# Kernel optimization log

Measured on AMD Instinct MI355X. Metric: run time of the kernel, lower is better.

Reference implementation:

```python
import jax, jax.numpy as jnp
import numpy as np

HIDDEN = 1024
HEADS = 16
CHUNK = 128
NEG_INF = -1e10  # matches source's -10000000000.0


def setup_inputs() -> dict:
    key = jax.random.key(0)
    k1, k2, k3 = jax.random.split(key, 3)
    B, S = 2, 4096
    x = jax.random.normal(k1, (B, S, HIDDEN), dtype=jnp.float32)
    w_qkv = jax.random.normal(k2, (HIDDEN, 3 * HIDDEN), dtype=jnp.float32) / np.sqrt(HIDDEN).astype(np.float32)
    w_out = jax.random.normal(k3, (HIDDEN, HIDDEN), dtype=jnp.float32) / np.sqrt(HIDDEN).astype(np.float32)
    return {"x": x, "w_qkv": w_qkv, "w_out": w_out}


def reference(x, w_qkv, w_out):
    B, S, _ = x.shape
    H, D = HEADS, HIDDEN // HEADS
    # fused qkv projection (flax Dense, no bias): [B,S,3,H,D]
    qkv = (x @ w_qkv).reshape(B, S, 3, H, D)
    q, k, v = qkv[:, :, 0], qkv[:, :, 1], qkv[:, :, 2]
    scale = jnp.sqrt(jnp.asarray(D, x.dtype))
    n_chunks = S // CHUNK
    # [n_chunks, B, CHUNK, H, D] query chunks; scan keeps only one chunk's
    # [B,H,CHUNK,S] score tensor live at a time (faithful to source's chunking).
    q_chunks = q.reshape(B, n_chunks, CHUNK, H, D).transpose(1, 0, 2, 3, 4)
    starts = jnp.arange(n_chunks) * CHUNK

    def step(carry, inp):
        qc, start = inp  # qc: [B,CHUNK,H,D]
        scores = jnp.einsum('bqhd,bkhd->bhqk', qc, k) / scale  # [B,H,CHUNK,S]
        causal = (jnp.arange(CHUNK)[:, None] + start) >= jnp.arange(S)[None, :]
        scores = jnp.where(causal[None, None], scores, NEG_INF)
        attn = jax.nn.softmax(scores, axis=-1)
        out_c = jnp.einsum('bhqk,bkhd->bqhd', attn, v).reshape(B, CHUNK, H * D)
        return carry, out_c

    _, outs = jax.lax.scan(step, None, (q_chunks, starts))  # [n,B,CHUNK,hidden]
    out = outs.transpose(1, 0, 2, 3).reshape(B, S, H * D)
    return out @ w_out
```

## Files before the change

kernel.cpp:

```cpp
#include <hip/hip_runtime.h>
#include <hip/hip_bf16.h>

#define SEQ 4096
#define BATCH 2
#define HEADS 16
#define DHEAD 64
#define HID 1024

typedef unsigned short ushort_t;
typedef unsigned int uint_t;
typedef __attribute__((ext_vector_type(8))) short short8;
typedef __attribute__((ext_vector_type(4))) float f32x4;
typedef __attribute__((ext_vector_type(16))) float f32x16;
typedef __attribute__((ext_vector_type(4))) uint_t u32x4;

__device__ __forceinline__ float exp2_fast(float x) {
  return __builtin_amdgcn_exp2f(x);
}

__device__ __forceinline__ float max3f(float a, float b, float c) {
  float r;
  asm("v_max3_f32 %0, %1, %2, %3" : "=v"(r) : "v"(a), "v"(b), "v"(c));
  return r;
}

__device__ __forceinline__ ushort_t f2b(float f) {
  unsigned u = __builtin_bit_cast(unsigned, f);
  unsigned r = 0x7fffu + ((u >> 16) & 1u);
  return (ushort_t)((u + r) >> 16);
}

__device__ __forceinline__ uint_t cvt_pk_bf16(float lo, float hi) {
  uint_t r;
  asm("v_cvt_pk_bf16_f32 %0, %1, %2" : "=v"(r) : "v"(lo), "v"(hi));
  return r;
}

__device__ __forceinline__ void permlane_swap(uint_t& a, uint_t& b) {
  asm("v_permlane32_swap_b32 %0, %1" : "+v"(a), "+v"(b));
}

__device__ __forceinline__ void gload16(const void* g, void* l) {
  __builtin_amdgcn_global_load_lds((const __attribute__((address_space(1))) void*)g,
                                   (__attribute__((address_space(3))) void*)l, 16, 0, 0);
}

__device__ __forceinline__ f32x4 mfma_bf16(short8 a, short8 b, f32x4 c) {
  return __builtin_amdgcn_mfma_f32_16x16x32_bf16(a, b, c, 0, 0, 0);
}

__device__ __forceinline__ f32x16 mfma32_bf16(short8 a, short8 b, f32x16 c) {
  return __builtin_amdgcn_mfma_f32_32x32x16_bf16(a, b, c, 0, 0, 0);
}

__global__ void cvt_kernel(const float* __restrict__ in, ushort_t* __restrict__ out, int n4) {
  int i = blockIdx.x * blockDim.x + threadIdx.x;
  if (i >= n4) return;
  float4 v = reinterpret_cast<const float4*>(in)[i];
  ushort4 o;
  o.x = f2b(v.x); o.y = f2b(v.y); o.z = f2b(v.z); o.w = f2b(v.w);
  reinterpret_cast<ushort4*>(out)[i] = o;
}

__global__ void transpose_cvt_kernel(const float* __restrict__ in, ushort_t* __restrict__ out,
                                     int rows, int cols) {
  __shared__ float tile[32][33];
  int tx = threadIdx.x & 31, ty = threadIdx.x >> 5;
  int r0 = blockIdx.y * 32, c0 = blockIdx.x * 32;
#pragma unroll
  for (int i = 0; i < 32; i += 8)
    tile[ty + i][tx] = in[(size_t)(r0 + ty + i) * cols + c0 + tx];
  __syncthreads();
#pragma unroll
  for (int i = 0; i < 32; i += 8)
    out[(size_t)(c0 + ty + i) * rows + r0 + tx] = f2b(tile[tx][ty + i]);
}

template <int MODE>
__global__ __launch_bounds__(256, 2)
void gemm_kernel(const ushort_t* __restrict__ A, const ushort_t* __restrict__ BT,
                 int M, int N, int K,
                 ushort_t* __restrict__ qg, ushort_t* __restrict__ kg,
                 ushort_t* __restrict__ vTg, float* __restrict__ outf) {
  __shared__ ushort_t lA[128 * 64];
  __shared__ ushort_t lB[128 * 64];
  int tid = threadIdx.x;
  int lane = tid & 63, w = tid >> 6;
  int m0 = blockIdx.x * 128, n0 = blockIdx.y * 128;
  int wr = (w >> 1) * 64, wc = (w & 1) * 64;
  int lr = lane & 15, lg = lane >> 4;

  const f32x4 z4 = {0.f, 0.f, 0.f, 0.f};
  f32x4 acc[4][4];
#pragma unroll
  for (int m = 0; m < 4; ++m)
#pragma unroll
    for (int n = 0; n < 4; ++n) acc[m][n] = z4;

  int ktiles = K >> 6;
  for (int kt = 0; kt < ktiles; ++kt) {
    int k0 = kt << 6;
#pragma unroll
    for (int i = 0; i < 4; ++i) {
      int c = i * 256 + tid;
      int row = c >> 3, cc = c & 7;
      gload16(A + (size_t)(m0 + row) * K + k0 + (cc ^ (row & 7)) * 8, lA + c * 8);
    }
#pragma unroll
    for (int i = 0; i < 4; ++i) {
      int c = i * 256 + tid;
      int row = c >> 3, cc = c & 7;
      gload16(BT + (size_t)(n0 + row) * K + k0 + (cc ^ (row & 7)) * 8, lB + c * 8);
    }
    __syncthreads();
#pragma unroll
    for (int kk = 0; kk < 2; ++kk) {
      short8 a[4], b[4];
#pragma unroll
      for (int m = 0; m < 4; ++m) {
        int row = wr + m * 16 + lr, cc = kk * 4 + lg;
        a[m] = *(const short8*)(lA + row * 64 + ((cc ^ (row & 7)) << 3));
      }
#pragma unroll
      for (int n = 0; n < 4; ++n) {
        int row = wc + n * 16 + lr, cc = kk * 4 + lg;
        b[n] = *(const short8*)(lB + row * 64 + ((cc ^ (row & 7)) << 3));
      }
      __builtin_amdgcn_s_setprio(1);
#pragma unroll
      for (int m = 0; m < 4; ++m)
#pragma unroll
        for (int n = 0; n < 4; ++n)
          acc[m][n] = mfma_bf16(a[m], b[n], acc[m][n]);
      __builtin_amdgcn_s_setprio(0);
    }
    __syncthreads();
  }

#pragma unroll
  for (int m = 0; m < 4; ++m)
#pragma unroll
    for (int n = 0; n < 4; ++n)
#pragma unroll
      for (int r = 0; r < 4; ++r) {
        int i = m0 + wr + m * 16 + lg * 4 + r;
        int j = n0 + wc + n * 16 + lr;
        float v = acc[m][n][r];
        if (MODE == 0) {
          int mat = j >> 10, rem = j & 1023;
          int h = rem >> 6, d = rem & 63;
          int b = i >> 12, s = i & 4095;
          int bh = b * HEADS + h;
          ushort_t val = f2b(mat == 0 ? v * 0.18033688f : v);
          if (mat == 0)      qg[((size_t)bh * SEQ + s) * DHEAD + d] = val;
          else if (mat == 1) kg[((size_t)bh * SEQ + s) * DHEAD + d] = val;
          else               vTg[((size_t)bh * DHEAD + d) * SEQ + s] = val;
        } else {
          outf[(size_t)i * N + j] = v;
        }
      }
}

struct QS {
  short8 qf[4];
  f32x16 o[2];
  f32x16 lacc;
  float mrow;
};

__device__ __forceinline__ void attn_qk_sm(int diag, int w, int l31, int hi, int lane,
                                           const ushort_t* lKc, QS& st, short8 (&pa)[8]) {
  f32x16 s[4];
#pragma unroll
  for (int t = 0; t < 4; ++t)
#pragma unroll
    for (int r = 0; r < 16; ++r) s[t][r] = 0.f;

#pragma unroll
  for (int t = 0; t < 4; ++t) {
    int row = t * 32 + l31;
#pragma unroll
    for (int kb = 0; kb < 4; ++kb) {
      int cc = kb * 2 + hi;
      short8 kf = *(const short8*)(lKc + row * 64 + ((cc ^ (row & 7)) << 3));
      __builtin_amdgcn_s_setprio(1);
      s[t] = mfma32_bf16(kf, st.qf[kb], s[t]);
      __builtin_amdgcn_s_setprio(0);
    }
  }

  if (diag) {
    int q = w * 32 + l31;
#pragma unroll
    for (int t = 0; t < 4; ++t)
#pragma unroll
      for (int r = 0; r < 16; ++r)
        if (t * 32 + (r & 3) + 8 * (r >> 2) + 4 * hi > q) s[t][r] = -1e30f;
  }

  float mx = fmaxf(s[0][0], s[0][1]);
#pragma unroll
  for (int t = 0; t < 4; ++t)
#pragma unroll
    for (int r = (t == 0 ? 2 : 0); r < 16; r += 2)
      mx = max3f(mx, s[t][r], s[t][r + 1]);
  mx = fmaxf(mx, __shfl_xor(mx, 32));
  float mo = st.mrow;
  if (!__all(mx - mo <= 8.0f)) {
    float mn = fmaxf(mo, mx);
    float al = exp2_fast(mo - mn);
    st.mrow = mn;
#pragma unroll
    for (int r = 0; r < 16; ++r) {
      float alo = __shfl(al, (r & 3) + 8 * (r >> 2) + 4 * hi);
      st.o[0][r] *= alo;
      st.o[1][r] *= alo;
      st.lacc[r] *= alo;
    }
  }
  float mloc = st.mrow;
#pragma unroll
  for (int t = 0; t < 4; ++t)
#pragma unroll
    for (int r = 0; r < 16; ++r)
      s[t][r] = exp2_fast(s[t][r] - mloc);

#pragma unroll
  for (int t = 0; t < 4; ++t) {
    uint_t w0 = cvt_pk_bf16(s[t][0], s[t][1]);
    uint_t w1 = cvt_pk_bf16(s[t][2], s[t][3]);
    uint_t w2 = cvt_pk_bf16(s[t][4], s[t][5]);
    uint_t w3 = cvt_pk_bf16(s[t][6], s[t][7]);
    permlane_swap(w0, w2);
    permlane_swap(w1, w3);
    u32x4 f0 = {w0, w1, w2, w3};
    pa[2 * t] = __builtin_bit_cast(short8, f0);
    uint_t w4 = cvt_pk_bf16(s[t][8], s[t][9]);
    uint_t w5 = cvt_pk_bf16(s[t][10], s[t][11]);
    uint_t w6 = cvt_pk_bf16(s[t][12], s[t][13]);
    uint_t w7 = cvt_pk_bf16(s[t][14], s[t][15]);
    permlane_swap(w4, w6);
    permlane_swap(w5, w7);
    u32x4 f1 = {w4, w5, w6, w7};
    pa[2 * t + 1] = __builtin_bit_cast(short8, f1);
  }
}

__device__ __forceinline__ void attn_pv(const ushort_t* lVc, int l31, int hi,
                                        const short8 (&pa)[8], const short8 ones8, QS& st) {
#pragma unroll
  for (int kb = 0; kb < 8; ++kb) {
    int cc = kb * 2 + hi;
    int row0 = l31, row1 = 32 + l31;
    short8 vf0 = *(const short8*)(lVc + row0 * 128 + ((cc ^ (row0 & 15)) << 3));
    short8 vf1 = *(const short8*)(lVc + row1 * 128 + ((cc ^ (row1 & 15)) << 3));
    __builtin_amdgcn_s_setprio(1);
    st.o[0] = mfma32_bf16(pa[kb], vf0, st.o[0]);
    st.lacc = mfma32_bf16(pa[kb], ones8, st.lacc);
    st.o[1] = mfma32_bf16(pa[kb], vf1, st.o[1]);
    __builtin_amdgcn_s_setprio(0);
  }
}

__device__ __forceinline__ void attn_epilogue(const QS& st, int q0, int bh,
                                              int w, int l31, int hi,
                                              ushort_t* __restrict__ og) {
  int b = bh >> 4, h = bh & 15;
#pragma unroll
  for (int r = 0; r < 16; ++r) {
    int qr = (r & 3) + 8 * (r >> 2) + 4 * hi;
    float inv = 1.0f / st.lacc[r];
    int srow = q0 + w * 32 + qr;
#pragma unroll
    for (int nd = 0; nd < 2; ++nd) {
      int col = h * 64 + nd * 32 + l31;
      og[((size_t)b * SEQ + srow) * HID + col] = f2b(st.o[nd][r] * inv);
    }
  }
}

__global__ __launch_bounds__(256, 2)
void attn_kernel(const ushort_t* __restrict__ qg, const ushort_t* __restrict__ kg,
                 const ushort_t* __restrict__ vTg, ushort_t* __restrict__ og) {
  __shared__ ushort_t lK[2][128 * 64];
  __shared__ ushort_t lV[64 * 128];

  int bid = blockIdx.x;
  int xcd = bid & 7, idx = bid >> 3;
  int bh = xcd * 4 + (idx & 3);
  int qt = 31 - (idx >> 2);
  int q0 = qt * 128;
  const ushort_t* Q = qg + (size_t)bh * SEQ * DHEAD;
  const ushort_t* Kp = kg + (size_t)bh * SEQ * DHEAD;
  const ushort_t* Vt = vTg + (size_t)bh * DHEAD * SEQ;

  int tid = threadIdx.x, lane = tid & 63, w = tid >> 6;
  int l31 = lane & 31, hi = lane >> 5;

  short8 ones8;
#pragma unroll
  for (int i = 0; i < 8; ++i) ones8[i] = (short)0x3F80;

#pragma unroll
  for (int i = 0; i < 4; ++i) {
    int c = i * 256 + tid;
    int row = c >> 3, cc = c & 7;
    size_t off = (cc ^ (row & 7)) * 8;
    gload16(Q + (size_t)(q0 + row) * DHEAD + off, &lV[c * 8]);
    gload16(Kp + (size_t)row * DHEAD + off, &lK[0][c * 8]);
  }
  __syncthreads();

  QS st;
  int qrow = w * 32 + l31;
#pragma unroll
  for (int kb = 0; kb < 4; ++kb) {
    int cc = kb * 2 + hi;
    st.qf[kb] = *(const short8*)(&lV[0] + qrow * 64 + ((cc ^ (qrow & 7)) << 3));
  }
  asm volatile("s_waitcnt lgkmcnt(0)");
  __syncthreads();

  st.mrow = -1e30f;
#pragma unroll
  for (int r = 0; r < 16; ++r) { st.o[0][r] = 0.f; st.o[1][r] = 0.f; st.lacc[r] = 0.f; }

  for (int jt = 0; jt <= qt; ++jt) {
    int cur = jt & 1, nxt = cur ^ 1;
#pragma unroll
    for (int i = 0; i < 4; ++i) {
      int c = i * 256 + tid;
      int d = c >> 4, cc = c & 15;
      gload16(Vt + (size_t)d * SEQ + jt * 128 + (cc ^ (d & 15)) * 8, &lV[c * 8]);
    }
    if (jt < qt) {
      int j0n = (jt + 1) * 128;
#pragma unroll
      for (int i = 0; i < 4; ++i) {
        int c = i * 256 + tid;
        int row = c >> 3, cc = c & 7;
        gload16(Kp + (size_t)(j0n + row) * DHEAD + (cc ^ (row & 7)) * 8, &lK[nxt][c * 8]);
      }
    }

    short8 pa[8];
    attn_qk_sm(jt == qt, w, l31, hi, lane, &lK[cur][0], st, pa);

    __syncthreads();
    attn_pv(&lV[0], l31, hi, pa, ones8, st);
    __syncthreads();
  }

  attn_epilogue(st, q0, bh, w, l31, hi, og);
}

extern "C" void kernel_launch(void* const* d_in, const int* in_sizes, int n_in,
                              void* d_out, int out_size, void* d_ws, size_t ws_size,
                              hipStream_t stream) {
  const float* x = (const float*)d_in[0];
  const float* wqkv = (const float*)d_in[1];
  const float* wout = (const float*)d_in[2];
  float* out = (float*)d_out;

  if (ws_size < 75497472u) return;

  char* ws = (char*)d_ws;
  ushort_t* xb    = (ushort_t*)(ws);
  ushort_t* wqkvT = (ushort_t*)(ws + 16777216);
  ushort_t* woutT = (ushort_t*)(ws + 23068672);
  ushort_t* qgb   = (ushort_t*)(ws + 25165824);
  ushort_t* kgb   = (ushort_t*)(ws + 41943040);
  ushort_t* vTb   = (ushort_t*)(ws + 58720256);
  ushort_t* ob    = xb;

  cvt_kernel<<<dim3(8192), dim3(256), 0, stream>>>(x, xb, 2097152);
  transpose_cvt_kernel<<<dim3(96, 32), dim3(256), 0, stream>>>(wqkv, wqkvT, 1024, 3072);
  transpose_cvt_kernel<<<dim3(32, 32), dim3(256), 0, stream>>>(wout, woutT, 1024, 1024);
  gemm_kernel<0><<<dim3(64, 24), dim3(256), 0, stream>>>(xb, wqkvT, 8192, 3072, 1024,
                                                         qgb, kgb, vTb, nullptr);
  attn_kernel<<<dim3(1024), dim3(256), 0, stream>>>(qgb, kgb, vTb, ob);
  gemm_kernel<1><<<dim3(64, 8), dim3(256), 0, stream>>>(ob, woutT, 8192, 1024, 1024,
                                                        nullptr, nullptr, nullptr, out);
}
```

Measured before the change: 218.3 us.

## Use 256x256 double-buffered pipelined GEMM for QKV projection

Replaces the 128x128 QKV projection GEMM with a 512-thread, 256x256-tile kernel. It double-buffers LDS, uses XOR-swizzled async global-to-LDS loads, and splits each k-tile into four quadrant phases so loads of the next tile overlap the MFMA work. The larger tile is meant to raise arithmetic intensity and hide memory latency. In exchange it needs more LDS, runs one block per CU, and launches only 384 blocks, which may leave CUs underused. The output GEMM moves into a separate kernel whose only job is writing the float32 result.

```diff
diff --git a/kernel.cpp b/kernel.cpp
--- a/kernel.cpp
+++ b/kernel.cpp
@@ -76,12 +76,130 @@
     out[(size_t)(c0 + ty + i) * rows + r0 + tx] = f2b(tile[tx][ty + i]);
 }
 
-template <int MODE>
+#define G256_PHASE(CUR, QM, QN)                                                     \
+  {                                                                                 \
+    short8 a[4][2], b[2][2];                                                        \
+    _Pragma("unroll") for (int f = 0; f < 4; ++f)                                   \
+        _Pragma("unroll") for (int kk = 0; kk < 2; ++kk) {                          \
+      int row = (QM) * 128 + wm * 64 + f * 16 + lr;                                 \
+      a[f][kk] = *(const short8*)(&lA[CUR][row * 64 + (((kk * 4 + lg) ^ (row & 7)) << 3)]); \
+    }                                                                               \
+    _Pragma("unroll") for (int g = 0; g < 2; ++g)                                   \
+        _Pragma("unroll") for (int kk = 0; kk < 2; ++kk) {                          \
+      int row = (QN) * 128 + wn * 32 + g * 16 + lr;                                 \
+      b[g][kk] = *(const short8*)(&lB[CUR][row * 64 + (((kk * 4 + lg) ^ (row & 7)) << 3)]); \
+    }                                                                               \
+    __builtin_amdgcn_s_setprio(1);                                                  \
+    _Pragma("unroll") for (int kk = 0; kk < 2; ++kk)                                \
+        _Pragma("unroll") for (int f = 0; f < 4; ++f)                               \
+            _Pragma("unroll") for (int g = 0; g < 2; ++g)                           \
+                acc[QM][QN][f][g] = mfma_bf16(a[f][kk], b[g][kk], acc[QM][QN][f][g]); \
+    __builtin_amdgcn_s_setprio(0);                                                  \
+  }
+
+#define G256_TOP()                                   \
+  asm volatile("s_waitcnt vmcnt(4)" ::: "memory");   \
+  __builtin_amdgcn_sched_barrier(0);                 \
+  __builtin_amdgcn_s_barrier();                      \
+  __builtin_amdgcn_sched_barrier(0);
+
+__global__ __launch_bounds__(512, 1)
+void gemm256_kernel(const ushort_t* __restrict__ A, const ushort_t* __restrict__ BT,
+                    int M, int N, int K,
+                    ushort_t* __restrict__ qg, ushort_t* __restrict__ kg,
+                    ushort_t* __restrict__ vTg) {
+  __shared__ ushort_t lA[2][256 * 64];
+  __shared__ ushort_t lB[2][256 * 64];
+
+  int tid = threadIdx.x;
+  int lane = tid & 63, wv = tid >> 6;
+  int wm = wv >> 2, wn = wv & 3;
+  int lr = lane & 15, lg = lane >> 4;
+  int m0 = blockIdx.x * 256, n0 = blockIdx.y * 256;
+  int nt = K >> 6;
+
+  const ushort_t* Ab = A + (size_t)m0 * K;
+  const ushort_t* Bb = BT + (size_t)n0 * K;
+
+  auto stageA = [&](int t, int h) {
+    int k0 = t << 6;
+#pragma unroll
+    for (int ld = 0; ld < 2; ++ld) {
+      int c = ld * 512 + tid;
+      int row = c >> 3, cc = c & 7;
+      gload16(Ab + (size_t)(h * 128 + row) * K + k0 + ((cc ^ (row & 7)) << 3),
+              &lA[t & 1][(h * 128 + row) * 64 + cc * 8]);
+    }
+  };
+  auto stageB = [&](int t, int h) {
+    int k0 = t << 6;
+#pragma unroll
+    for (int ld = 0; ld < 2; ++ld) {
+      int c = ld * 512 + tid;
+      int row = c >> 3, cc = c & 7;
+      gload16(Bb + (size_t)(h * 128 + row) * K + k0 + ((cc ^ (row & 7)) << 3),
+              &lB[t & 1][(h * 128 + row) * 64 + cc * 8]);
+    }
+  };
+
+  f32x4 acc[2][2][4][2];
+  const f32x4 z4 = {0.f, 0.f, 0.f, 0.f};
+#pragma unroll
+  for (int qm = 0; qm < 2; ++qm)
+#pragma unroll
+    for (int qn = 0; qn < 2; ++qn)
+#pragma unroll
+      for (int f = 0; f < 4; ++f)
+#pragma unroll
+        for (int g = 0; g < 2; ++g) acc[qm][qn][f][g] = z4;
+
+  stageA(0, 0); stageB(0, 0);
+  stageA(0, 1); stageB(0, 1);
+  stageA(1, 0); stageB(1, 0);
+
+  for (int T = 0; T < nt; ++T) {
+    int cur = T & 1;
+    G256_TOP();
+    if (T + 1 < nt) stageA(T + 1, 1);
+    G256_PHASE(cur, 0, 0);
+    G256_TOP();
+    if (T + 1 < nt) stageB(T + 1, 1);
+    G256_PHASE(cur, 0, 1);
+    G256_TOP();
+    if (T + 2 < nt) stageA(T + 2, 0);
+    G256_PHASE(cur, 1, 0);
+    G256_TOP();
+    if (T + 2 < nt) stageB(T + 2, 0);
+    G256_PHASE(cur, 1, 1);
+  }
+
+#pragma unroll
+  for (int qm = 0; qm < 2; ++qm)
+#pragma unroll
+    for (int qn = 0; qn < 2; ++qn)
+#pragma unroll
+      for (int f = 0; f < 4; ++f)
+#pragma unroll
+        for (int g = 0; g < 2; ++g)
+#pragma unroll
+          for (int r = 0; r < 4; ++r) {
+            int i = m0 + qm * 128 + wm * 64 + f * 16 + lg * 4 + r;
+            int j = n0 + qn * 128 + wn * 32 + g * 16 + lr;
+            int mat = j >> 10, rem = j & 1023;
+            int h = rem >> 6, d = rem & 63;
+            int b = i >> 12, s = i & 4095;
+            int bh = b * HEADS + h;
+            float v = acc[qm][qn][f][g][r];
+            ushort_t val = f2b(mat == 0 ? v * 0.18033688f : v);
+            if (mat == 0)      qg[((size_t)bh * SEQ + s) * DHEAD + d] = val;
+            else if (mat == 1) kg[((size_t)bh * SEQ + s) * DHEAD + d] = val;
+            else               vTg[((size_t)bh * DHEAD + d) * SEQ + s] = val;
+          }
+}
+
 __global__ __launch_bounds__(256, 2)
-void gemm_kernel(const ushort_t* __restrict__ A, const ushort_t* __restrict__ BT,
-                 int M, int N, int K,
-                 ushort_t* __restrict__ qg, ushort_t* __restrict__ kg,
-                 ushort_t* __restrict__ vTg, float* __restrict__ outf) {
+void gemm_out_kernel(const ushort_t* __restrict__ A, const ushort_t* __restrict__ BT,
+                     int M, int N, int K, float* __restrict__ outf) {
   __shared__ ushort_t lA[128 * 64];
   __shared__ ushort_t lB[128 * 64];
   int tid = threadIdx.x;
@@ -145,19 +263,7 @@
       for (int r = 0; r < 4; ++r) {
         int i = m0 + wr + m * 16 + lg * 4 + r;
         int j = n0 + wc + n * 16 + lr;
-        float v = acc[m][n][r];
-        if (MODE == 0) {
-          int mat = j >> 10, rem = j & 1023;
-          int h = rem >> 6, d = rem & 63;
-          int b = i >> 12, s = i & 4095;
-          int bh = b * HEADS + h;
-          ushort_t val = f2b(mat == 0 ? v * 0.18033688f : v);
-          if (mat == 0)      qg[((size_t)bh * SEQ + s) * DHEAD + d] = val;
-          else if (mat == 1) kg[((size_t)bh * SEQ + s) * DHEAD + d] = val;
-          else               vTg[((size_t)bh * DHEAD + d) * SEQ + s] = val;
-        } else {
-          outf[(size_t)i * N + j] = v;
-        }
+        outf[(size_t)i * N + j] = acc[m][n][r];
       }
 }
 
@@ -376,9 +482,8 @@
   cvt_kernel<<<dim3(8192), dim3(256), 0, stream>>>(x, xb, 2097152);
   transpose_cvt_kernel<<<dim3(96, 32), dim3(256), 0, stream>>>(wqkv, wqkvT, 1024, 3072);
   transpose_cvt_kernel<<<dim3(32, 32), dim3(256), 0, stream>>>(wout, woutT, 1024, 1024);
-  gemm_kernel<0><<<dim3(64, 24), dim3(256), 0, stream>>>(xb, wqkvT, 8192, 3072, 1024,
-                                                         qgb, kgb, vTb, nullptr);
+  gemm256_kernel<<<dim3(32, 12), dim3(512), 0, stream>>>(xb, wqkvT, 8192, 3072, 1024,
+                                                         qgb, kgb, vTb);
   attn_kernel<<<dim3(1024), dim3(256), 0, stream>>>(qgb, kgb, vTb, ob);
-  gemm_kernel<1><<<dim3(64, 8), dim3(256), 0, stream>>>(ob, woutT, 8192, 1024, 1024,
-                                                        nullptr, nullptr, nullptr, out);
-}
+  gemm_out_kernel<<<dim3(64, 8), dim3(256), 0, stream>>>(ob, woutT, 8192, 1024, 1024, out);
+}
```

Result: slower. 253.5 us (+16.1%).
